# Kernel optimization log

Hardware: AMD Instinct MI355X
Metric: run time of the kernel (lower is better)

The kernel has to match this reference:

```python
import jax, jax.numpy as jnp
import numpy as np

B, N, FIN, FOUT = 32, 1024, 128, 128
NEG_SLOPE = 0.01  # torch nn.LeakyReLU default


def setup_inputs() -> dict:
    key = jax.random.key(0)
    k1, k2, k3, k4 = jax.random.split(key, 4)
    node_mat = jax.random.normal(k1, (B, N, FIN), dtype=jnp.float32)
    adj_mat = jax.random.uniform(k2, (B, N, N), dtype=jnp.float32)
    # nn.Linear(FIN, FOUT): weight [FOUT, FIN], bias [FOUT]
    bound = 1.0 / np.sqrt(FIN)
    W = jax.random.uniform(k3, (FOUT, FIN), minval=-bound, maxval=bound, dtype=jnp.float32)
    b = jax.random.uniform(k4, (FOUT,), minval=-bound, maxval=bound, dtype=jnp.float32)
    return {"node_mat": node_mat, "adj_mat": adj_mat, "W": W, "b": b}


def reference(node_mat, adj_mat, W, b):
    # degree per node: row-sum of adjacency [B, N, 1]
    n_neighbors = adj_mat.sum(axis=-1, keepdims=True)
    # D^-1 A : the original builds eye*(1/deg) then bmm; algebraically a row scaling
    norm_adj = adj_mat / n_neighbors                      # [B, N, N]
    agg = jnp.einsum('bnm,bmf->bnf', norm_adj, node_mat)  # [B, N, FIN]
    out = jnp.einsum('bnf,of->bno', agg, W) + b           # [B, N, FOUT]
    return jnp.where(out >= 0, out, NEG_SLOPE * out)      # LeakyReLU
```

## Files before the change

### kernel.cpp

```cpp
#include <hip/hip_runtime.h>
#include <cstdint>
#include <cstddef>

#define BB   32
#define NN   1024
#define FIN  128
#define FOUT 128

typedef __attribute__((ext_vector_type(8))) short bf16x8;
typedef __attribute__((ext_vector_type(4))) float f32x4;

__device__ __forceinline__ unsigned int f2bf(float f) {
    union { float f; unsigned int u; } v; v.f = f;
    unsigned int u = v.u;
    return (u + 0x7FFFu + ((u >> 16) & 1u)) >> 16;
}
__device__ __forceinline__ unsigned int pack2(float a, float b) {
    return f2bf(a) | (f2bf(b) << 16);
}

__device__ __forceinline__ void load_lds16(const void* g, void* l) {
    __builtin_amdgcn_global_load_lds(
        (const __attribute__((address_space(1))) unsigned int*)g,
        (__attribute__((address_space(3))) unsigned int*)l, 16, 0, 0);
}

__global__ __launch_bounds__(256) void y_kernel(const float* __restrict__ node,
                                                const float* __restrict__ W,
                                                unsigned short* __restrict__ Yt) {
    __shared__ unsigned short Wlds[128 * 136];
    __shared__ unsigned short Nlds[64 * 136];

    const int tid = threadIdx.x;
    const int bid = blockIdx.x;
    const int b   = bid >> 4;
    const int m0  = (bid & 15) * 64;

    #pragma unroll
    for (int i = 0; i < 16; ++i) {
        const int idx = i * 256 + tid;
        const int row = idx >> 5;
        const int c   = (idx & 31) * 4;
        float4 v = ((const float4*)W)[idx];
        uint2 p; p.x = pack2(v.x, v.y); p.y = pack2(v.z, v.w);
        *(uint2*)&Wlds[row * 136 + c] = p;
    }
    {
        const float* base = node + ((size_t)b * NN + m0) * FIN;
        #pragma unroll
        for (int i = 0; i < 8; ++i) {
            const int idx = i * 256 + tid;
            const int row = idx >> 5;
            const int c   = (idx & 31) * 4;
            float4 v = *(const float4*)(base + row * FIN + c);
            uint2 p; p.x = pack2(v.x, v.y); p.y = pack2(v.z, v.w);
            *(uint2*)&Nlds[row * 136 + c] = p;
        }
    }
    __syncthreads();

    const int w = tid >> 6, lane = tid & 63;
    const int wo = w * 32;
    const int lcol = lane & 15, lk = (lane >> 4) * 8;

    f32x4 acc[2][4] = {};
    #pragma unroll
    for (int kc = 0; kc < 4; ++kc) {
        const int kof = kc * 32 + lk;
        bf16x8 a[2], bb[4];
        #pragma unroll
        for (int mi = 0; mi < 2; ++mi)
            a[mi] = *(const bf16x8*)&Wlds[(wo + mi*16 + lcol) * 136 + kof];
        #pragma unroll
        for (int ni = 0; ni < 4; ++ni)
            bb[ni] = *(const bf16x8*)&Nlds[(ni*16 + lcol) * 136 + kof];
        #pragma unroll
        for (int mi = 0; mi < 2; ++mi)
            #pragma unroll
            for (int ni = 0; ni < 4; ++ni)
                acc[mi][ni] = __builtin_amdgcn_mfma_f32_16x16x32_bf16(
                    a[mi], bb[ni], acc[mi][ni], 0, 0, 0);
    }
    __syncthreads();

    unsigned short* Ylds = Wlds;
    const int rq = (lane >> 4) * 4;
    #pragma unroll
    for (int mi = 0; mi < 2; ++mi)
        #pragma unroll
        for (int ni = 0; ni < 4; ++ni)
            #pragma unroll
            for (int r = 0; r < 4; ++r) {
                const int o = wo + mi * 16 + rq + r;
                const int m = ni * 16 + lcol;
                Ylds[o * 72 + m] = (unsigned short)f2bf(acc[mi][ni][r]);
            }
    __syncthreads();

    {
        const int oq = tid >> 3, c = (tid & 7) * 8;
        #pragma unroll
        for (int j = 0; j < 4; ++j) {
            const int o = oq + 32 * j;
            uint4 v = *(const uint4*)&Ylds[o * 72 + c];
            *(uint4*)(Yt + ((size_t)b * FOUT + o) * NN + m0 + c) = v;
        }
    }
}

__global__ __launch_bounds__(256, 4) void gcn_kernel(const float* __restrict__ adj,
                                                     const unsigned short* __restrict__ Yt,
                                                     const float* __restrict__ bias,
                                                     float* __restrict__ out) {
    __shared__ char smem[24576 + 128];
    float* Afp          = (float*)smem;
    float* Clds         = (float*)smem;
    float* rs           = (float*)(smem + 24576);

    const int tid  = threadIdx.x;
    const int lane = tid & 63;
    const int w    = tid >> 6;
    const int bid  = blockIdx.x;
    const int b    = bid >> 5;
    const int n0   = (bid & 31) * 32;

    const float* aSrc[2];
    char*        aDst[2];
    #pragma unroll
    for (int j = 0; j < 2; ++j) {
        const int s = (w * 2 + j) * 64 + lane;
        const int r = s >> 4, c = s & 15;
        const int g = c ^ (r & 7);
        aSrc[j] = adj + ((size_t)(b * NN + n0 + r)) * NN + g * 4;
        aDst[j] = smem + (w * 2 + j) * 1024;
    }
    const unsigned short* bSrc[4];
    char*                 bDst[4];
    #pragma unroll
    for (int j = 0; j < 4; ++j) {
        const int s = (w * 4 + j) * 64 + lane;
        const int o = s >> 3, c = s & 7;
        const int g = c ^ (o & 7);
        bSrc[j] = Yt + ((size_t)(b * FOUT + o)) * NN + g * 8;
        bDst[j] = smem + 8192 + (w * 4 + j) * 1024;
    }

    const int lcol = lane & 15, q = lane >> 4;
    const int wm = (w & 1) * 16, wn = (w >> 1) * 64;
    const int key = lcol & 7;

    int offA[2][2], offB[2][4];
    #pragma unroll
    for (int kc = 0; kc < 2; ++kc) {
        const int gA = kc * 8 + q * 2;
        const int R  = wm + lcol;
        offA[kc][0] = (R * 64 + ((gA    ) ^ key) * 4) * 4;
        offA[kc][1] = (R * 64 + ((gA + 1) ^ key) * 4) * 4;
        #pragma unroll
        for (int ni = 0; ni < 4; ++ni) {
            const int Rb = wn + ni * 16 + lcol;
            const int gB = kc * 4 + q;
            offB[kc][ni] = 8192 + (Rb * 32 + (gB ^ key) * 4) * 4;
        }
    }

    float bcol[4];
    #pragma unroll
    for (int ni = 0; ni < 4; ++ni) bcol[ni] = bias[wn + ni * 16 + lcol];

    f32x4 acc[4] = {};
    float rsum = 0.f;

    for (int s = 0; s < 16; ++s) {
        #pragma unroll
        for (int j = 0; j < 2; ++j) load_lds16(aSrc[j] + s * 64, aDst[j]);
        #pragma unroll
        for (int j = 0; j < 4; ++j) load_lds16(bSrc[j] + s * 64, bDst[j]);
        __syncthreads();

        #pragma unroll
        for (int kc = 0; kc < 2; ++kc) {
            const float4 f0 = *(const float4*)(smem + offA[kc][0]);
            const float4 f1 = *(const float4*)(smem + offA[kc][1]);
            rsum += ((f0.x + f0.y) + (f0.z + f0.w)) + ((f1.x + f1.y) + (f1.z + f1.w));
            uint4 pk;
            pk.x = pack2(f0.x, f0.y); pk.y = pack2(f0.z, f0.w);
            pk.z = pack2(f1.x, f1.y); pk.w = pack2(f1.z, f1.w);
            const bf16x8 a = *(const bf16x8*)&pk;
            #pragma unroll
            for (int ni = 0; ni < 4; ++ni) {
                const bf16x8 bb = *(const bf16x8*)(smem + offB[kc][ni]);
                acc[ni] = __builtin_amdgcn_mfma_f32_16x16x32_bf16(a, bb, acc[ni], 0, 0, 0);
            }
        }
        __syncthreads();
    }

    rsum += __shfl_xor(rsum, 16);
    rsum += __shfl_xor(rsum, 32);
    if (w < 2) rs[wm + lcol] = rsum;
    __syncthreads();

    const int rq = q * 4;
    float sc[4];
    #pragma unroll
    for (int r = 0; r < 4; ++r) sc[r] = 1.0f / rs[wm + rq + r];
    #pragma unroll
    for (int ni = 0; ni < 4; ++ni) {
        const int col = wn + ni * 16 + lcol;
        #pragma unroll
        for (int r = 0; r < 4; ++r) {
            const int row = wm + rq + r;
            float v = acc[ni][r] * sc[r] + bcol[ni];
            v = (v >= 0.f) ? v : 0.01f * v;
            Clds[row * 132 + col] = v;
        }
    }
    __syncthreads();

    {
        float* outB = out + ((size_t)(b * NN + n0)) * FOUT;
        #pragma unroll
        for (int i = 0; i < 4; ++i) {
            const int idx = i * 256 + tid;
            const int row = idx >> 5;
            const int c4  = (idx & 31) * 4;
            *(float4*)(outB + (size_t)row * FOUT + c4) = *(const float4*)&Clds[row * 132 + c4];
        }
    }
}

extern "C" void kernel_launch(void* const* d_in, const int* in_sizes, int n_in,
                              void* d_out, int out_size, void* d_ws, size_t ws_size,
                              hipStream_t stream) {
    const float* node = (const float*)d_in[0];
    const float* adj  = (const float*)d_in[1];
    const float* W    = (const float*)d_in[2];
    const float* bias = (const float*)d_in[3];
    float* out = (float*)d_out;
    unsigned short* Yt = (unsigned short*)d_ws;

    hipLaunchKernelGGL(y_kernel,   dim3(512),  dim3(256), 0, stream, node, W, Yt);
    hipLaunchKernelGGL(gcn_kernel, dim3(1024), dim3(256), 0, stream, adj, Yt, bias, out);
}
```

Baseline: 226.2 us.

## Double-buffer LDS tiles in gcn_kernel and store output directly from registers

Double-buffers the LDS staging area so the global-to-LDS loads for the next K step are issued before computing on the current buffer, with manual vmcnt waits and barriers in place of two __syncthreads per step. It also drops the LDS row-sum exchange in favour of a wave shuffle, and writes outputs straight from registers instead of going through an LDS transpose. The aim is to hide adjacency-load latency in this memory-bound kernel. In exchange, LDS use doubles to 48KB and the occupancy hint of 4 blocks is dropped, which may lower occupancy, and the direct stores are less coalesced.

```diff
diff --git a/kernel.cpp b/kernel.cpp
--- a/kernel.cpp
+++ b/kernel.cpp
@@ -108,14 +108,11 @@
     }
 }
 
-__global__ __launch_bounds__(256, 4) void gcn_kernel(const float* __restrict__ adj,
-                                                     const unsigned short* __restrict__ Yt,
-                                                     const float* __restrict__ bias,
-                                                     float* __restrict__ out) {
-    __shared__ char smem[24576 + 128];
-    float* Afp          = (float*)smem;
-    float* Clds         = (float*)smem;
-    float* rs           = (float*)(smem + 24576);
+__global__ __launch_bounds__(256) void gcn_kernel(const float* __restrict__ adj,
+                                                  const unsigned short* __restrict__ Yt,
+                                                  const float* __restrict__ bias,
+                                                  float* __restrict__ out) {
+    __shared__ char smem[2 * 24576];
 
     const int tid  = threadIdx.x;
     const int lane = tid & 63;
@@ -124,108 +121,105 @@
     const int b    = bid >> 5;
     const int n0   = (bid & 31) * 32;
 
-    const float* aSrc[2];
-    char*        aDst[2];
+    const int lcol = lane & 15, q = lane >> 4;
+    const int wm = (w & 1) * 16, wn = (w >> 1) * 64;
+    const int key = lcol & 7;
+
+    const float* aSrc[2]; int aOff[2];
     #pragma unroll
     for (int j = 0; j < 2; ++j) {
         const int s = (w * 2 + j) * 64 + lane;
         const int r = s >> 4, c = s & 15;
         const int g = c ^ (r & 7);
         aSrc[j] = adj + ((size_t)(b * NN + n0 + r)) * NN + g * 4;
-        aDst[j] = smem + (w * 2 + j) * 1024;
-    }
-    const unsigned short* bSrc[4];
-    char*                 bDst[4];
+        aOff[j] = (w * 2 + j) * 1024;
+    }
+    const unsigned short* bSrcp[4]; int bOff[4];
     #pragma unroll
     for (int j = 0; j < 4; ++j) {
         const int s = (w * 4 + j) * 64 + lane;
         const int o = s >> 3, c = s & 7;
         const int g = c ^ (o & 7);
-        bSrc[j] = Yt + ((size_t)(b * FOUT + o)) * NN + g * 8;
-        bDst[j] = smem + 8192 + (w * 4 + j) * 1024;
-    }
-
-    const int lcol = lane & 15, q = lane >> 4;
-    const int wm = (w & 1) * 16, wn = (w >> 1) * 64;
-    const int key = lcol & 7;
+        bSrcp[j] = Yt + ((size_t)(b * FOUT + o)) * NN + g * 8;
+        bOff[j] = 8192 + (w * 4 + j) * 1024;
+    }
 
     int offA[2][2], offB[2][4];
     #pragma unroll
     for (int kc = 0; kc < 2; ++kc) {
         const int gA = kc * 8 + q * 2;
         const int R  = wm + lcol;
-        offA[kc][0] = (R * 64 + ((gA    ) ^ key) * 4) * 4;
-        offA[kc][1] = (R * 64 + ((gA + 1) ^ key) * 4) * 4;
+        offA[kc][0] = R * 256 + (( gA     ) ^ key) * 16;
+        offA[kc][1] = R * 256 + (( gA + 1 ) ^ key) * 16;
         #pragma unroll
         for (int ni = 0; ni < 4; ++ni) {
             const int Rb = wn + ni * 16 + lcol;
             const int gB = kc * 4 + q;
-            offB[kc][ni] = 8192 + (Rb * 32 + (gB ^ key) * 4) * 4;
-        }
-    }
-
-    float bcol[4];
-    #pragma unroll
-    for (int ni = 0; ni < 4; ++ni) bcol[ni] = bias[wn + ni * 16 + lcol];
+            offB[kc][ni] = 8192 + Rb * 128 + (gB ^ key) * 16;
+        }
+    }
 
     f32x4 acc[4] = {};
     float rsum = 0.f;
 
-    for (int s = 0; s < 16; ++s) {
-        #pragma unroll
-        for (int j = 0; j < 2; ++j) load_lds16(aSrc[j] + s * 64, aDst[j]);
-        #pragma unroll
-        for (int j = 0; j < 4; ++j) load_lds16(bSrc[j] + s * 64, bDst[j]);
-        __syncthreads();
-
+    auto compute = [&](const char* cb) {
         #pragma unroll
         for (int kc = 0; kc < 2; ++kc) {
-            const float4 f0 = *(const float4*)(smem + offA[kc][0]);
-            const float4 f1 = *(const float4*)(smem + offA[kc][1]);
-            rsum += ((f0.x + f0.y) + (f0.z + f0.w)) + ((f1.x + f1.y) + (f1.z + f1.w));
+            const float4 f0 = *(const float4*)(cb + offA[kc][0]);
+            const float4 f1 = *(const float4*)(cb + offA[kc][1]);
+            rsum += ((f0.x + f0.y) + (f0.z + f0.w))
+                  + ((f1.x + f1.y) + (f1.z + f1.w));
             uint4 pk;
             pk.x = pack2(f0.x, f0.y); pk.y = pack2(f0.z, f0.w);
             pk.z = pack2(f1.x, f1.y); pk.w = pack2(f1.z, f1.w);
-            const bf16x8 a = *(const bf16x8*)&pk;
+            const bf16x8 af = *(const bf16x8*)&pk;
             #pragma unroll
             for (int ni = 0; ni < 4; ++ni) {
-                const bf16x8 bb = *(const bf16x8*)(smem + offB[kc][ni]);
-                acc[ni] = __builtin_amdgcn_mfma_f32_16x16x32_bf16(a, bb, acc[ni], 0, 0, 0);
+                const bf16x8 bb = *(const bf16x8*)(cb + offB[kc][ni]);
+                acc[ni] = __builtin_amdgcn_mfma_f32_16x16x32_bf16(af, bb, acc[ni], 0, 0, 0);
             }
         }
-        __syncthreads();
-    }
+    };
+
+    #pragma unroll
+    for (int j = 0; j < 2; ++j) load_lds16(aSrc[j], smem + aOff[j]);
+    #pragma unroll
+    for (int j = 0; j < 4; ++j) load_lds16(bSrcp[j], smem + bOff[j]);
+
+    for (int s = 0; s < 15; ++s) {
+        char*       nb = smem + ((s + 1) & 1) * 24576;
+        const char* cb = smem + ( s      & 1) * 24576;
+        #pragma unroll
+        for (int j = 0; j < 2; ++j) load_lds16(aSrc[j] + (s + 1) * 64, nb + aOff[j]);
+        #pragma unroll
+        for (int j = 0; j < 4; ++j) load_lds16(bSrcp[j] + (s + 1) * 64, nb + bOff[j]);
+
+        asm volatile("s_waitcnt vmcnt(6)\n\ts_barrier" ::: "memory");
+        compute(cb);
+        asm volatile("s_waitcnt lgkmcnt(0)\n\ts_barrier" ::: "memory");
+    }
+
+    asm volatile("s_waitcnt vmcnt(0)\n\ts_barrier" ::: "memory");
+    compute(smem + 24576);
 
     rsum += __shfl_xor(rsum, 16);
     rsum += __shfl_xor(rsum, 32);
-    if (w < 2) rs[wm + lcol] = rsum;
-    __syncthreads();
-
-    const int rq = q * 4;
+
     float sc[4];
     #pragma unroll
-    for (int r = 0; r < 4; ++r) sc[r] = 1.0f / rs[wm + rq + r];
+    for (int r = 0; r < 4; ++r) sc[r] = 1.0f / __shfl(rsum, q * 4 + r);
+    float bcol[4];
+    #pragma unroll
+    for (int ni = 0; ni < 4; ++ni) bcol[ni] = bias[wn + ni * 16 + lcol];
+
+    float* outB = out + ((size_t)(b * NN + n0 + wm)) * FOUT;
     #pragma unroll
     for (int ni = 0; ni < 4; ++ni) {
-        const int col = wn + ni * 16 + lcol;
         #pragma unroll
         for (int r = 0; r < 4; ++r) {
-            const int row = wm + rq + r;
             float v = acc[ni][r] * sc[r] + bcol[ni];
             v = (v >= 0.f) ? v : 0.01f * v;
-            Clds[row * 132 + col] = v;
-        }
-    }
-    __syncthreads();
-
-    {
-        float* outB = out + ((size_t)(b * NN + n0)) * FOUT;
-        #pragma unroll
-        for (int i = 0; i < 4; ++i) {
-            const int idx = i * 256 + tid;
-            const int row = idx >> 5;
-            const int c4  = (idx & 31) * 4;
-            *(float4*)(outB + (size_t)row * FOUT + c4) = *(const float4*)&Clds[row * 132 + c4];
+            outB[(size_t)(q * 4 + r) * FOUT + wn + ni * 16 + lcol] = v;
         }
     }
 }
```

Result: no change. 230.6 us (+1.9%).
